# Kernel tuning notes

Measured on AMD Instinct MI355X. Metric: run time of the kernel, lower is better.

Reference implementation:

```python
import jax, jax.numpy as jnp
import numpy as np

N_NODES = 50000
N_EDGES = 800000
FEAT = 64
HID = 128
N_TYPES = 4
N_REL = 3
N_LAYERS = 2
LN_EPS = 1e-5


def setup_inputs() -> dict:
    key = jax.random.key(0)
    ks = jax.random.split(key, 20)
    inp = {
        "z": jax.random.randint(ks[0], (N_NODES,), 0, 100, dtype=jnp.int32),
        "node_type": jax.random.randint(ks[1], (N_NODES,), 0, N_TYPES, dtype=jnp.int32),
        "edge_index": jax.random.randint(ks[2], (2, N_EDGES), 0, N_NODES, dtype=jnp.int32),
        "edge_type": jax.random.randint(ks[3], (N_EDGES,), 0, N_REL, dtype=jnp.int32),
        # learned parameters
        "z_embed": jax.random.normal(ks[4], (100, FEAT), jnp.float32),
        "enc_w1": jax.random.normal(ks[5], (N_TYPES, FEAT, HID), jnp.float32) * 0.05,
        "enc_b1": jnp.zeros((N_TYPES, HID), jnp.float32),
        "enc_w2": jax.random.normal(ks[6], (N_TYPES, HID, HID), jnp.float32) * 0.05,
        "enc_b2": jnp.zeros((N_TYPES, HID), jnp.float32),
        "lin_w": jax.random.normal(ks[7], (N_LAYERS, HID, HID), jnp.float32) * 0.05,
        "lin_b": jnp.zeros((N_LAYERS, HID), jnp.float32),
        "rel_w": jax.random.normal(ks[8], (N_LAYERS, N_REL, HID, HID), jnp.float32) * 0.05,
        "ln_g": jnp.ones((N_LAYERS, HID), jnp.float32),
        "ln_b": jnp.zeros((N_LAYERS, HID), jnp.float32),
        "reg_w": jax.random.normal(ks[9], (HID, 1), jnp.float32) * 0.05,
        "reg_b": jnp.zeros((1,), jnp.float32),
    }
    return inp


def _layer_norm(x, g, b):
    mu = jnp.mean(x, axis=-1, keepdims=True)
    var = jnp.mean((x - mu) ** 2, axis=-1, keepdims=True)
    return (x - mu) * jax.lax.rsqrt(var + LN_EPS) * g + b


def reference(z, node_type, edge_index, edge_type, z_embed, enc_w1, enc_b1,
              enc_w2, enc_b2, lin_w, lin_b, rel_w, ln_g, ln_b, reg_w, reg_b):
    n = z.shape[0]
    # FeatureBuilder (site_ads=None path): atomic-number embedding lookup
    raw = z_embed[z]  # [N, FEAT]
    # TypeSpecificEncoder: run all 4 type MLPs, select per node by node_type
    h = jax.nn.relu(jnp.einsum('nd,tdh->nth', raw, enc_w1) + enc_b1)  # [N,T,H]
    enc_all = jnp.einsum('nth,tho->nto', h, enc_w2) + enc_b2           # [N,T,H]
    x = jnp.take_along_axis(enc_all, node_type[:, None, None].astype(jnp.int32), axis=1)[:, 0, :]

    src, dst = edge_index[0], edge_index[1]
    deg = jax.ops.segment_sum(jnp.ones((edge_type.shape[0],), x.dtype), dst, num_segments=n)
    deg = jnp.clip(deg, 1.0, None)[:, None]  # [N,1]

    for l in range(N_LAYERS):
        out = jnp.zeros_like(x)
        x_src = x[src]  # [E, H] gathered source features
        for r in range(N_REL):
            mask = (edge_type == r).astype(x.dtype)[:, None]
            msg = (x_src * mask) @ rel_w[l, r]  # [E, H]
            out = out + jax.ops.segment_sum(msg, dst, num_segments=n)
        out = out / deg
        x = _layer_norm(x @ lin_w[l] + lin_b[l] + out, ln_g[l], ln_b[l])

    pooled = jnp.mean(x, axis=0)  # mean pooling, mask = all ones
    return pooled @ reg_w + reg_b  # [1]
```

## Files before the change

### kernel.cpp

```cpp
#include <hip/hip_runtime.h>

#define N_NODES 50000
#define N_EDGES 800000
#define FEAT 64
#define HID 128
#define N_TYPES 4
#define N_REL 3
#define N_LAYERS 2
#define LN_EPS 1e-5f
#define NROWS 50016
#define NG32 1563
#define CAP 64
#define NBKT 196
#define CAP1 4608
#define EPB 4096
#define BINCAP 56
#define NCOMBO 400
#define WT_STRIDE 136

typedef __attribute__((ext_vector_type(8))) short bf16x8;
typedef __attribute__((ext_vector_type(16))) float f32x16;
typedef __attribute__((ext_vector_type(2))) float f32x2;

static __device__ inline unsigned short f2bf(float f) {
    unsigned int u = __float_as_uint(f);
    return (unsigned short)((u + 0x7fffu + ((u >> 16) & 1u)) >> 16);
}
static __device__ inline unsigned int packbf2(float lo, float hi) {
    return (unsigned int)f2bf(lo) | ((unsigned int)f2bf(hi) << 16);
}

static __device__ inline void acc8_fp8(float* a, uint2 w) {
    f32x2 d0 = __builtin_amdgcn_cvt_pk_f32_fp8((int)w.x, false);
    f32x2 d1 = __builtin_amdgcn_cvt_pk_f32_fp8((int)w.x, true);
    f32x2 d2 = __builtin_amdgcn_cvt_pk_f32_fp8((int)w.y, false);
    f32x2 d3 = __builtin_amdgcn_cvt_pk_f32_fp8((int)w.y, true);
    a[0] += d0[0]; a[1] += d0[1]; a[2] += d1[0]; a[3] += d1[1];
    a[4] += d2[0]; a[5] += d2[1]; a[6] += d3[0]; a[7] += d3[1];
}
static __device__ inline bf16x8 f8_to_bf16x8(uint2 w) {
    f32x2 d0 = __builtin_amdgcn_cvt_pk_f32_fp8((int)w.x, false);
    f32x2 d1 = __builtin_amdgcn_cvt_pk_f32_fp8((int)w.x, true);
    f32x2 d2 = __builtin_amdgcn_cvt_pk_f32_fp8((int)w.y, false);
    f32x2 d3 = __builtin_amdgcn_cvt_pk_f32_fp8((int)w.y, true);
    union { bf16x8 v; unsigned int u[4]; } r;
    r.u[0] = packbf2(d0[0], d0[1]);
    r.u[1] = packbf2(d1[0], d1[1]);
    r.u[2] = packbf2(d2[0], d2[1]);
    r.u[3] = packbf2(d3[0], d3[1]);
    return r.v;
}

__global__ __launch_bounds__(256) void build_tables_kernel(
    const int* __restrict__ src, const int* __restrict__ dst,
    const int* __restrict__ et, const int* __restrict__ z,
    const int* __restrict__ nt,
    const float* __restrict__ z_embed, const float* __restrict__ w1,
    const float* __restrict__ b1, const float* __restrict__ w2,
    const float* __restrict__ b2, const float* __restrict__ rel_w,
    const float* __restrict__ lin_w, const float* __restrict__ lin_b,
    unsigned short* __restrict__ combo, int* __restrict__ bcnt,
    int* __restrict__ bucket, unsigned int* __restrict__ ytab,
    float* __restrict__ lintab, unsigned short* __restrict__ wbuf,
    float* __restrict__ pooled) {
    __shared__ int lbin[NBKT * BINCAP];
    __shared__ int lcnt[NBKT];
    __shared__ int lbase[NBKT];
    __shared__ float h[HID];
    __shared__ float xrow[HID];
    __shared__ float tmp[HID];

    int b = blockIdx.x;
    if (b < NBKT) {
        int ci = b * 256 + threadIdx.x;
        if (ci < N_NODES) combo[ci] = (unsigned short)(z[ci] * 4 + nt[ci]);
        for (int i = threadIdx.x; i < NBKT; i += 256) lcnt[i] = 0;
        __syncthreads();
        int base = b * EPB;
#pragma unroll
        for (int i = 0; i < EPB / 256; ++i) {
            int e = base + i * 256 + threadIdx.x;
            if (e < N_EDGES) {
                int d = dst[e];
                int bk = d >> 8;
                int v = src[e] | (et[e] << 16) | ((d & 255) << 18);
                int pos = atomicAdd(&lcnt[bk], 1);
                if (pos < BINCAP) lbin[bk * BINCAP + pos] = v;
            }
        }
        __syncthreads();
        if (threadIdx.x < NBKT) {
            int c = min(lcnt[threadIdx.x], BINCAP);
            lcnt[threadIdx.x] = c;
            lbase[threadIdx.x] = atomicAdd(&bcnt[threadIdx.x], c);
        }
        __syncthreads();
        int wv = threadIdx.x >> 6, ln = threadIdx.x & 63;
        for (int bb = wv; bb < NBKT; bb += 4) {
            int c = lcnt[bb];
            if (ln < c) {
                int gp = lbase[bb] + ln;
                if (gp < CAP1) bucket[bb * CAP1 + gp] = lbin[bb * BINCAP + ln];
            }
        }
        return;
    }
    if (b >= NBKT + NCOMBO) {
        int pb = b - (NBKT + NCOMBO);
        if (pb == 0 && threadIdx.x < HID) pooled[threadIdx.x] = 0.0f;
        int idx = pb * 256 + threadIdx.x;
        int k = idx & 127;
        int col = (idx >> 7) & 127;
        int mat = idx >> 14;
        float w = (mat < 3) ? rel_w[(((size_t)(3 + mat)) * HID + k) * HID + col]
                            : lin_w[((size_t)(HID + k)) * HID + col];
        wbuf[(size_t)mat * HID * WT_STRIDE + col * WT_STRIDE + k] = f2bf(w);
        return;
    }
    int c = b - NBKT;
    int zi = c >> 2;
    int t = c & 3;
    int j = threadIdx.x;
    bool act = j < HID;
    if (act) {
        float acc = b1[t * HID + j];
#pragma unroll 8
        for (int k = 0; k < FEAT; ++k)
            acc = fmaf(z_embed[zi * FEAT + k], w1[((size_t)t * FEAT + k) * HID + j], acc);
        h[j] = fmaxf(acc, 0.0f);
    }
    __syncthreads();
    if (act) {
        float acc2 = b2[t * HID + j];
#pragma unroll 8
        for (int k = 0; k < HID; ++k)
            acc2 = fmaf(h[k], w2[(size_t)t * HID * HID + k * HID + j], acc2);
        xrow[j] = acc2;
    }
    __syncthreads();
#pragma unroll 1
    for (int r = 0; r < N_REL; ++r) {
        if (act) {
            float a = 0.f;
            const float* W = rel_w + (size_t)r * HID * HID;
#pragma unroll 8
            for (int k = 0; k < HID; ++k) a = fmaf(xrow[k], W[k * HID + j], a);
            tmp[j] = a;
        }
        __syncthreads();
        if (j < 32) {
            int w0 = __builtin_amdgcn_cvt_pk_fp8_f32(tmp[4 * j], tmp[4 * j + 1], 0, false);
            w0 = __builtin_amdgcn_cvt_pk_fp8_f32(tmp[4 * j + 2], tmp[4 * j + 3], w0, true);
            ytab[(r * NCOMBO + c) * 32 + j] = (unsigned)w0;
        }
        __syncthreads();
    }
    if (act) {
        float a = lin_b[j];
#pragma unroll 8
        for (int k = 0; k < HID; ++k) a = fmaf(xrow[k], lin_w[k * HID + j], a);
        lintab[c * HID + j] = a;
    }
}

__global__ __launch_bounds__(256) void build2_kernel(const int* __restrict__ bcnt,
                                                     const int* __restrict__ bucket,
                                                     const unsigned short* __restrict__ combo,
                                                     int* __restrict__ cnt3,
                                                     int* __restrict__ payload) {
    __shared__ int lcnt[256 * 3];
    for (int i = threadIdx.x; i < 768; i += 256) lcnt[i] = 0;
    __syncthreads();
    int b = blockIdx.x;
    int n0 = b << 8;
    int cb = min(bcnt[b], CAP1);
    const int* bk = bucket + b * CAP1;
    for (int i = threadIdx.x; i < cb; i += 256) {
        int v = bk[i];
        atomicAdd(&lcnt[((v >> 18) & 255) * 3 + ((v >> 16) & 3)], 1);
    }
    __syncthreads();
    int t = threadIdx.x;
    int c0 = min(lcnt[t * 3 + 0], CAP);
    int c1 = min(lcnt[t * 3 + 1], CAP - c0);
    int c2 = min(lcnt[t * 3 + 2], CAP - c0 - c1);
    __syncthreads();
    lcnt[t * 3 + 0] = 0;
    lcnt[t * 3 + 1] = c0;
    lcnt[t * 3 + 2] = c0 + c1;
    int node = n0 + t;
    if (node < N_NODES) cnt3[node] = c0 | (c1 << 8) | (c2 << 16);
    __syncthreads();
    for (int i = threadIdx.x; i < cb; i += 256) {
        int v = bk[i];
        int dl = (v >> 18) & 255;
        int r = (v >> 16) & 3;
        int sc = v & 0xffff;
        int pos = atomicAdd(&lcnt[dl * 3 + r], 1);
        if (pos < CAP)
            payload[((n0 + dl) << 6) + pos] = sc | ((int)combo[sc] << 18);
    }
}

__global__ __launch_bounds__(256) void gather_ln1_kernel(
    const int* __restrict__ cnt3, const int* __restrict__ payload,
    const uint2* __restrict__ ytab8, const float* __restrict__ lintab,
    const unsigned short* __restrict__ combo, const float* __restrict__ lng,
    const float* __restrict__ lnb, uint2* __restrict__ xf8) {
    int tid = blockIdx.x * 256 + threadIdx.x;
    int node = tid >> 4;
    int l16 = tid & 15;
    int c3 = cnt3[node];
    int c0 = c3 & 255, c1 = (c3 >> 8) & 255, c2 = (c3 >> 16) & 255;
    int tot = c0 + c1 + c2;
    float inv = 1.0f / (float)max(tot, 1);
    const int* pl = payload + (node << 6);
    float a[8] = {};
    int e = 0;
#pragma unroll 1
    for (int r = 0; r < 3; ++r) {
        int e1 = (r == 0) ? c0 : (r == 1) ? c0 + c1 : tot;
        int base = (r * NCOMBO) << 4;
        for (; e + 4 <= e1; e += 4) {
            int pA = pl[e], pB = pl[e + 1], pC = pl[e + 2], pD = pl[e + 3];
            uint2 vA = ytab8[base + ((pA >> 18) << 4) + l16];
            uint2 vB = ytab8[base + ((pB >> 18) << 4) + l16];
            uint2 vC = ytab8[base + ((pC >> 18) << 4) + l16];
            uint2 vD = ytab8[base + ((pD >> 18) << 4) + l16];
            acc8_fp8(a, vA);
            acc8_fp8(a, vB);
            acc8_fp8(a, vC);
            acc8_fp8(a, vD);
        }
        if (e + 2 <= e1) {
            int pA = pl[e], pB = pl[e + 1];
            uint2 vA = ytab8[base + ((pA >> 18) << 4) + l16];
            uint2 vB = ytab8[base + ((pB >> 18) << 4) + l16];
            acc8_fp8(a, vA);
            acc8_fp8(a, vB);
            e += 2;
        }
        if (e < e1) {
            int p = pl[e]; ++e;
            acc8_fp8(a, ytab8[base + ((p >> 18) << 4) + l16]);
        }
    }
    const float* lrow = lintab + (int)combo[node] * HID + l16 * 8;
    float v[8], s = 0.f, q = 0.f;
#pragma unroll
    for (int j = 0; j < 8; ++j) {
        v[j] = fmaf(a[j], inv, lrow[j]);
        s += v[j];
        q += v[j] * v[j];
    }
#pragma unroll
    for (int mk = 1; mk < 16; mk <<= 1) {
        s += __shfl_xor(s, mk);
        q += __shfl_xor(q, mk);
    }
    float mu = s * (1.0f / HID);
    float rstd = rsqrtf(q * (1.0f / HID) - mu * mu + LN_EPS);
    const float* g8 = lng + l16 * 8;
    const float* b8 = lnb + l16 * 8;
    float o[8];
#pragma unroll
    for (int j = 0; j < 8; ++j) o[j] = (v[j] - mu) * rstd * g8[j] + b8[j];
    int lo = 0, hi = 0;
    lo = __builtin_amdgcn_cvt_pk_fp8_f32(o[0], o[1], lo, false);
    lo = __builtin_amdgcn_cvt_pk_fp8_f32(o[2], o[3], lo, true);
    hi = __builtin_amdgcn_cvt_pk_fp8_f32(o[4], o[5], hi, false);
    hi = __builtin_amdgcn_cvt_pk_fp8_f32(o[6], o[7], hi, true);
    xf8[(node << 4) + l16] = make_uint2((unsigned)lo, (unsigned)hi);
}

__global__ __launch_bounds__(256) void gather3_kernel(const int* __restrict__ cnt3,
                                                      const int* __restrict__ payload,
                                                      const uint2* __restrict__ xf8,
                                                      uint2* __restrict__ s0,
                                                      uint2* __restrict__ s1,
                                                      uint2* __restrict__ s2) {
    int tid = blockIdx.x * 256 + threadIdx.x;
    int node = tid >> 4;
    int l16 = tid & 15;
    int c3 = cnt3[node];
    int c0 = c3 & 255, c1 = (c3 >> 8) & 255, c2 = (c3 >> 16) & 255;
    int tot = c0 + c1 + c2;
    float inv = 1.0f / (float)max(tot, 1);
    const int* pl = payload + (node << 6);
    int o = node * 16 + l16;
    int e = 0;
#pragma unroll 1
    for (int r = 0; r < 3; ++r) {
        int e1 = (r == 0) ? c0 : (r == 1) ? c0 + c1 : tot;
        float a[8] = {};
        for (; e + 4 <= e1; e += 4) {
            int pA = pl[e], pB = pl[e + 1], pC = pl[e + 2], pD = pl[e + 3];
            uint2 vA = xf8[((pA & 0xffff) << 4) + l16];
            uint2 vB = xf8[((pB & 0xffff) << 4) + l16];
            uint2 vC = xf8[((pC & 0xffff) << 4) + l16];
            uint2 vD = xf8[((pD & 0xffff) << 4) + l16];
            acc8_fp8(a, vA);
            acc8_fp8(a, vB);
            acc8_fp8(a, vC);
            acc8_fp8(a, vD);
        }
        if (e + 2 <= e1) {
            int pA = pl[e], pB = pl[e + 1];
            uint2 vA = xf8[((pA & 0xffff) << 4) + l16];
            uint2 vB = xf8[((pB & 0xffff) << 4) + l16];
            acc8_fp8(a, vA);
            acc8_fp8(a, vB);
            e += 2;
        }
        if (e < e1) {
            int p = pl[e]; ++e;
            acc8_fp8(a, xf8[((p & 0xffff) << 4) + l16]);
        }
        int lo = 0, hi = 0;
        lo = __builtin_amdgcn_cvt_pk_fp8_f32(a[0] * inv, a[1] * inv, lo, false);
        lo = __builtin_amdgcn_cvt_pk_fp8_f32(a[2] * inv, a[3] * inv, lo, true);
        hi = __builtin_amdgcn_cvt_pk_fp8_f32(a[4] * inv, a[5] * inv, hi, false);
        hi = __builtin_amdgcn_cvt_pk_fp8_f32(a[6] * inv, a[7] * inv, hi, true);
        uint2 w = make_uint2((unsigned)lo, (unsigned)hi);
        if (r == 0) s0[o] = w;
        else if (r == 1) s1[o] = w;
        else s2[o] = w;
    }
}

__global__ __launch_bounds__(512) void fused_layer_kernel(
    const uint2* __restrict__ s0, const uint2* __restrict__ s1,
    const uint2* __restrict__ s2, const uint2* __restrict__ xf8,
    const uint4* __restrict__ wbuf, const float* __restrict__ lb,
    const float* __restrict__ lng, const float* __restrict__ lnb,
    float* __restrict__ pooled, const float* __restrict__ reg_w,
    const float* __restrict__ reg_b, float* __restrict__ out,
    int* __restrict__ done) {
    __shared__ __align__(16) unsigned short Wt[4 * HID * WT_STRIDE];
    __shared__ float csh[3 * HID];
    __shared__ float pooled_sh[HID];
    __shared__ int lastFlag;

    int wave = threadIdx.x >> 6;
    int lane = threadIdx.x & 63;
    int n32 = lane & 31;
    int hf = lane >> 5;

    int g0 = wave * gridDim.x + blockIdx.x;
    bool active = g0 < NG32;
    int rbase = active ? ((g0 * 32 + n32) * 16 + hf) : 0;

    uint2 bufA[8], bufB[8];
    {
        const uint2* p0 = s0 + rbase;
#pragma unroll
        for (int t = 0; t < 8; ++t) bufA[t] = p0[t * 2];
    }

    if (threadIdx.x < HID) {
        pooled_sh[threadIdx.x] = 0.0f;
        csh[threadIdx.x] = lb[threadIdx.x];
        csh[HID + threadIdx.x] = lng[threadIdx.x];
        csh[2 * HID + threadIdx.x] = lnb[threadIdx.x];
    }
    uint4* wt4 = (uint4*)Wt;
#pragma unroll
    for (int i = 0; i < 17; ++i)
        wt4[i * 512 + threadIdx.x] = wbuf[i * 512 + threadIdx.x];
    __syncthreads();

    float pacc[4] = {0.f, 0.f, 0.f, 0.f};

    if (active) {
        f32x16 acc[4];
#pragma unroll
        for (int ct = 0; ct < 4; ++ct)
#pragma unroll
            for (int i = 0; i < 16; ++i) acc[ct][i] = 0.0f;

        const unsigned short* wbase = Wt + n32 * WT_STRIDE + hf * 8;

#define DOMAT(buf, m)                                                          \
        {                                                                      \
            const unsigned short* wm = wbase + (m) * (HID * WT_STRIDE);        \
            _Pragma("unroll")                                                  \
            for (int t = 0; t < 8; ++t) {                                      \
                bf16x8 afr = f8_to_bf16x8(buf[t]);                             \
                _Pragma("unroll")                                              \
                for (int ct = 0; ct < 4; ++ct) {                               \
                    bf16x8 bfr = *(const bf16x8*)(wm + ct * 32 * WT_STRIDE + t * 16); \
                    acc[ct] = __builtin_amdgcn_mfma_f32_32x32x16_bf16(         \
                        afr, bfr, acc[ct], 0, 0, 0);                           \
                }                                                              \
            }                                                                  \
        }
#define LDMAT(buf, srcp)                                                       \
        {                                                                      \
            const uint2* _p = (srcp) + rbase;                                  \
            _Pragma("unroll")                                                  \
            for (int t = 0; t < 8; ++t) buf[t] = _p[t * 2];                    \
        }

        LDMAT(bufB, s1);
        DOMAT(bufA, 0);
        LDMAT(bufA, s2);
        DOMAT(bufB, 1);
        LDMAT(bufB, xf8);
        DOMAT(bufA, 2);
        DOMAT(bufB, 3);
#undef DOMAT
#undef LDMAT

        int node0 = g0 * 32;
#pragma unroll
        for (int reg = 0; reg < 16; ++reg) {
            int row = node0 + (reg & 3) + 8 * (reg >> 2) + 4 * hf;
            float v[4];
            float s = 0.f, q = 0.f;
#pragma unroll
            for (int ct = 0; ct < 4; ++ct) {
                v[ct] = acc[ct][reg] + csh[ct * 32 + n32];
                s += v[ct];
                q += v[ct] * v[ct];
            }
#pragma unroll
            for (int mk = 1; mk < 32; mk <<= 1) {
                s += __shfl_xor(s, mk);
                q += __shfl_xor(q, mk);
            }
            float mu = s * (1.0f / HID);
            float rstd = rsqrtf(q * (1.0f / HID) - mu * mu + LN_EPS);
            if (row < N_NODES) {
#pragma unroll
                for (int ct = 0; ct < 4; ++ct) {
                    int col = ct * 32 + n32;
                    pacc[ct] += (v[ct] - mu) * rstd * csh[HID + col] + csh[2 * HID + col];
                }
            }
        }
    }

#pragma unroll
    for (int ct = 0; ct < 4; ++ct) {
        float t = pacc[ct] + __shfl_xor(pacc[ct], 32);
        if (hf == 0) atomicAdd(&pooled_sh[ct * 32 + n32], t);
    }
    __syncthreads();
    if (threadIdx.x < HID) atomicAdd(&pooled[threadIdx.x], pooled_sh[threadIdx.x]);

    __threadfence();
    __syncthreads();
    if (threadIdx.x == 0)
        lastFlag = (atomicAdd(done, 1) == (int)gridDim.x - 1);
    __syncthreads();
    if (lastFlag && threadIdx.x < 64) {
        int l = threadIdx.x;
        float s = atomicAdd(&pooled[l], 0.0f) * reg_w[l] +
                  atomicAdd(&pooled[64 + l], 0.0f) * reg_w[64 + l];
#pragma unroll
        for (int o = 32; o; o >>= 1) s += __shfl_down(s, o);
        if (l == 0) out[0] = s * (1.0f / N_NODES) + reg_b[0];
    }
}

extern "C" void kernel_launch(void* const* d_in, const int* in_sizes, int n_in,
                              void* d_out, int out_size, void* d_ws, size_t ws_size,
                              hipStream_t stream) {
    const int* z = (const int*)d_in[0];
    const int* nt = (const int*)d_in[1];
    const int* ei = (const int*)d_in[2];
    const int* et = (const int*)d_in[3];
    const float* z_embed = (const float*)d_in[4];
    const float* enc_w1 = (const float*)d_in[5];
    const float* enc_b1 = (const float*)d_in[6];
    const float* enc_w2 = (const float*)d_in[7];
    const float* enc_b2 = (const float*)d_in[8];
    const float* lin_w = (const float*)d_in[9];
    const float* lin_b = (const float*)d_in[10];
    const float* rel_w = (const float*)d_in[11];
    const float* ln_g = (const float*)d_in[12];
    const float* ln_b = (const float*)d_in[13];
    const float* reg_w = (const float*)d_in[14];
    const float* reg_b = (const float*)d_in[15];
    float* out = (float*)d_out;

    const size_t NHf8 = (size_t)NROWS * HID;
    char* p = (char*)d_ws;
    uint2* xf8 = (uint2*)p;                     p += NHf8;
    uint2* s0 = (uint2*)p;                      p += NHf8;
    uint2* s1 = (uint2*)p;                      p += NHf8;
    uint2* s2 = (uint2*)p;                      p += NHf8;
    unsigned short* wbuf = (unsigned short*)p;  p += (size_t)4 * HID * WT_STRIDE * 2;
    unsigned int* ytab = (unsigned int*)p;      p += (size_t)N_REL * NCOMBO * HID;
    float* lintab = (float*)p;                  p += NCOMBO * HID * 4;
    unsigned short* combo = (unsigned short*)p; p += N_NODES * 2;
    float* pooled = (float*)p;                  p += HID * 4;
    int* cnt3 = (int*)p;                        p += N_NODES * 4;
    int* bcnt = (int*)p;                        p += NBKT * 4;
    int* done = (int*)p;                        p += 4;
    int* bucket = (int*)p;                      p += (size_t)NBKT * CAP1 * 4;
    int* payload = (int*)p;                     p += (size_t)N_NODES * CAP * 4;

    const int* src = ei;
    const int* dst = ei + N_EDGES;

    hipMemsetAsync(bcnt, 0, (NBKT + 1) * sizeof(int), stream);

    build_tables_kernel<<<NBKT + NCOMBO + 256, 256, 0, stream>>>(
        src, dst, et, z, nt, z_embed, enc_w1, enc_b1, enc_w2, enc_b2,
        rel_w, lin_w, lin_b, combo, bcnt, bucket, ytab, lintab, wbuf, pooled);

    build2_kernel<<<NBKT, 256, 0, stream>>>(bcnt, bucket, combo, cnt3, payload);

    gather_ln1_kernel<<<3125, 256, 0, stream>>>(cnt3, payload, (const uint2*)ytab, lintab,
                                                combo, ln_g, ln_b, xf8);
    gather3_kernel<<<3125, 256, 0, stream>>>(cnt3, payload, xf8, s0, s1, s2);
    fused_layer_kernel<<<256, 512, 0, stream>>>(
        s0, s1, s2, xf8, (const uint4*)wbuf, lin_b + HID, ln_g + HID, ln_b + HID,
        pooled, reg_w, reg_b, out, done);
}
```

Baseline: 230.2 us.

## Permute fp8 row layout for 16-byte loads and read weights from global

```diff
diff --git a/kernel.cpp b/kernel.cpp
--- a/kernel.cpp
+++ b/kernel.cpp
@@ -270,7 +270,8 @@
     lo = __builtin_amdgcn_cvt_pk_fp8_f32(o[2], o[3], lo, true);
     hi = __builtin_amdgcn_cvt_pk_fp8_f32(o[4], o[5], hi, false);
     hi = __builtin_amdgcn_cvt_pk_fp8_f32(o[6], o[7], hi, true);
-    xf8[(node << 4) + l16] = make_uint2((unsigned)lo, (unsigned)hi);
+    int slot = (l16 >> 1) + ((l16 & 1) << 3);
+    xf8[(node << 4) + slot] = make_uint2((unsigned)lo, (unsigned)hi);
 }
 
 __global__ __launch_bounds__(256) void gather3_kernel(const int* __restrict__ cnt3,
@@ -282,12 +283,13 @@
     int tid = blockIdx.x * 256 + threadIdx.x;
     int node = tid >> 4;
     int l16 = tid & 15;
+    int slot = (l16 >> 1) + ((l16 & 1) << 3);
     int c3 = cnt3[node];
     int c0 = c3 & 255, c1 = (c3 >> 8) & 255, c2 = (c3 >> 16) & 255;
     int tot = c0 + c1 + c2;
     float inv = 1.0f / (float)max(tot, 1);
     const int* pl = payload + (node << 6);
-    int o = node * 16 + l16;
+    int o = node * 16 + slot;
     int e = 0;
 #pragma unroll 1
     for (int r = 0; r < 3; ++r) {
@@ -295,10 +297,10 @@
         float a[8] = {};
         for (; e + 4 <= e1; e += 4) {
             int pA = pl[e], pB = pl[e + 1], pC = pl[e + 2], pD = pl[e + 3];
-            uint2 vA = xf8[((pA & 0xffff) << 4) + l16];
-            uint2 vB = xf8[((pB & 0xffff) << 4) + l16];
-            uint2 vC = xf8[((pC & 0xffff) << 4) + l16];
-            uint2 vD = xf8[((pD & 0xffff) << 4) + l16];
+            uint2 vA = xf8[((pA & 0xffff) << 4) + slot];
+            uint2 vB = xf8[((pB & 0xffff) << 4) + slot];
+            uint2 vC = xf8[((pC & 0xffff) << 4) + slot];
+            uint2 vD = xf8[((pD & 0xffff) << 4) + slot];
             acc8_fp8(a, vA);
             acc8_fp8(a, vB);
             acc8_fp8(a, vC);
@@ -306,15 +308,15 @@
         }
         if (e + 2 <= e1) {
             int pA = pl[e], pB = pl[e + 1];
-            uint2 vA = xf8[((pA & 0xffff) << 4) + l16];
-            uint2 vB = xf8[((pB & 0xffff) << 4) + l16];
+            uint2 vA = xf8[((pA & 0xffff) << 4) + slot];
+            uint2 vB = xf8[((pB & 0xffff) << 4) + slot];
             acc8_fp8(a, vA);
             acc8_fp8(a, vB);
             e += 2;
         }
         if (e < e1) {
             int p = pl[e]; ++e;
-            acc8_fp8(a, xf8[((p & 0xffff) << 4) + l16]);
+            acc8_fp8(a, xf8[((p & 0xffff) << 4) + slot]);
         }
         int lo = 0, hi = 0;
         lo = __builtin_amdgcn_cvt_pk_fp8_f32(a[0] * inv, a[1] * inv, lo, false);
@@ -329,14 +331,13 @@
 }
 
 __global__ __launch_bounds__(512) void fused_layer_kernel(
-    const uint2* __restrict__ s0, const uint2* __restrict__ s1,
-    const uint2* __restrict__ s2, const uint2* __restrict__ xf8,
-    const uint4* __restrict__ wbuf, const float* __restrict__ lb,
+    const uint4* __restrict__ s0, const uint4* __restrict__ s1,
+    const uint4* __restrict__ s2, const uint4* __restrict__ xf8,
+    const unsigned short* __restrict__ wbuf, const float* __restrict__ lb,
     const float* __restrict__ lng, const float* __restrict__ lnb,
     float* __restrict__ pooled, const float* __restrict__ reg_w,
     const float* __restrict__ reg_b, float* __restrict__ out,
     int* __restrict__ done) {
-    __shared__ __align__(16) unsigned short Wt[4 * HID * WT_STRIDE];
     __shared__ float csh[3 * HID];
     __shared__ float pooled_sh[HID];
     __shared__ int lastFlag;
@@ -348,13 +349,14 @@
 
     int g0 = wave * gridDim.x + blockIdx.x;
     bool active = g0 < NG32;
-    int rbase = active ? ((g0 * 32 + n32) * 16 + hf) : 0;
-
-    uint2 bufA[8], bufB[8];
+    int abase = active ? ((g0 * 32 + n32) * 8 + hf * 4) : 0;
+
+    uint4 bufA[4], bufB[4];
     {
-        const uint2* p0 = s0 + rbase;
-#pragma unroll
-        for (int t = 0; t < 8; ++t) bufA[t] = p0[t * 2];
+        const uint4* p0 = s0 + abase;
+        const uint4* p1 = s1 + abase;
+#pragma unroll
+        for (int i = 0; i < 4; ++i) { bufA[i] = p0[i]; bufB[i] = p1[i]; }
     }
 
     if (threadIdx.x < HID) {
@@ -363,10 +365,6 @@
         csh[HID + threadIdx.x] = lng[threadIdx.x];
         csh[2 * HID + threadIdx.x] = lnb[threadIdx.x];
     }
-    uint4* wt4 = (uint4*)Wt;
-#pragma unroll
-    for (int i = 0; i < 17; ++i)
-        wt4[i * 512 + threadIdx.x] = wbuf[i * 512 + threadIdx.x];
     __syncthreads();
 
     float pacc[4] = {0.f, 0.f, 0.f, 0.f};
@@ -378,14 +376,16 @@
 #pragma unroll
             for (int i = 0; i < 16; ++i) acc[ct][i] = 0.0f;
 
-        const unsigned short* wbase = Wt + n32 * WT_STRIDE + hf * 8;
+        const unsigned short* wlane = wbuf + n32 * WT_STRIDE + hf * 8;
 
 #define DOMAT(buf, m)                                                          \
         {                                                                      \
-            const unsigned short* wm = wbase + (m) * (HID * WT_STRIDE);        \
+            const unsigned short* wm = wlane + (size_t)(m) * (HID * WT_STRIDE);\
             _Pragma("unroll")                                                  \
             for (int t = 0; t < 8; ++t) {                                      \
-                bf16x8 afr = f8_to_bf16x8(buf[t]);                             \
+                uint2 f = (t & 1) ? make_uint2(buf[t >> 1].z, buf[t >> 1].w)   \
+                                  : make_uint2(buf[t >> 1].x, buf[t >> 1].y);  \
+                bf16x8 afr = f8_to_bf16x8(f);                                  \
                 _Pragma("unroll")                                              \
                 for (int ct = 0; ct < 4; ++ct) {                               \
                     bf16x8 bfr = *(const bf16x8*)(wm + ct * 32 * WT_STRIDE + t * 16); \
@@ -396,12 +396,11 @@
         }
 #define LDMAT(buf, srcp)                                                       \
         {                                                                      \
-            const uint2* _p = (srcp) + rbase;                                  \
+            const uint4* _p = (srcp) + abase;                                  \
             _Pragma("unroll")                                                  \
-            for (int t = 0; t < 8; ++t) buf[t] = _p[t * 2];                    \
-        }
-
-        LDMAT(bufB, s1);
+            for (int i = 0; i < 4; ++i) buf[i] = _p[i];                        \
+        }
+
         DOMAT(bufA, 0);
         LDMAT(bufA, s2);
         DOMAT(bufB, 1);
@@ -443,7 +442,7 @@
 #pragma unroll
     for (int ct = 0; ct < 4; ++ct) {
         float t = pacc[ct] + __shfl_xor(pacc[ct], 32);
-        if (hf == 0) atomicAdd(&pooled_sh[ct * 32 + n32], t);
+        if (hf == 0 && t != 0.0f) atomicAdd(&pooled_sh[ct * 32 + n32], t);
     }
     __syncthreads();
     if (threadIdx.x < HID) atomicAdd(&pooled[threadIdx.x], pooled_sh[threadIdx.x]);
@@ -515,7 +514,8 @@
     gather_ln1_kernel<<<3125, 256, 0, stream>>>(cnt3, payload, (const uint2*)ytab, lintab,
                                                 combo, ln_g, ln_b, xf8);
     gather3_kernel<<<3125, 256, 0, stream>>>(cnt3, payload, xf8, s0, s1, s2);
-    fused_layer_kernel<<<256, 512, 0, stream>>>(
-        s0, s1, s2, xf8, (const uint4*)wbuf, lin_b + HID, ln_g + HID, ln_b + HID,
+    fused_layer_kernel<<<784, 512, 0, stream>>>(
+        (const uint4*)s0, (const uint4*)s1, (const uint4*)s2, (const uint4*)xf8,
+        wbuf, lin_b + HID, ln_g + HID, ln_b + HID,
         pooled, reg_w, reg_b, out, done);
 }
```

After: 331.2 us. 1.44x slower.

## Switch final layer to 16x16x32 MFMA tiles with two groups per wave

Applied to the files above, without the earlier changes.

```diff
diff --git a/kernel.cpp b/kernel.cpp
--- a/kernel.cpp
+++ b/kernel.cpp
@@ -9,7 +9,7 @@
 #define N_LAYERS 2
 #define LN_EPS 1e-5f
 #define NROWS 50016
-#define NG32 1563
+#define NG16 3125
 #define CAP 64
 #define NBKT 196
 #define CAP1 4608
@@ -19,7 +19,7 @@
 #define WT_STRIDE 136
 
 typedef __attribute__((ext_vector_type(8))) short bf16x8;
-typedef __attribute__((ext_vector_type(16))) float f32x16;
+typedef __attribute__((ext_vector_type(4))) float f32x4;
 typedef __attribute__((ext_vector_type(2))) float f32x2;
 
 static __device__ inline unsigned short f2bf(float f) {
@@ -343,19 +343,25 @@
 
     int wave = threadIdx.x >> 6;
     int lane = threadIdx.x & 63;
-    int n32 = lane & 31;
-    int hf = lane >> 5;
+    int c16 = lane & 15;
+    int kg = lane >> 4;
 
     int g0 = wave * gridDim.x + blockIdx.x;
-    bool active = g0 < NG32;
-    int rbase = active ? ((g0 * 32 + n32) * 16 + hf) : 0;
-
-    uint2 bufA[8], bufB[8];
-    {
-        const uint2* p0 = s0 + rbase;
-#pragma unroll
-        for (int t = 0; t < 8; ++t) bufA[t] = p0[t * 2];
-    }
+    uint2 buf[16];
+
+#define LDALL(g)                                                               \
+    {                                                                          \
+        int _b = ((g) * 16 + c16) * 16 + kg;  \
+        _Pragma("unroll")                                                      \
+        for (int kk = 0; kk < 4; ++kk) {                                       \
+            buf[0 * 4 + kk] = s0[_b + kk * 4];                                 \
+            buf[1 * 4 + kk] = s1[_b + kk * 4];                                 \
+            buf[2 * 4 + kk] = s2[_b + kk * 4];                                 \
+            buf[3 * 4 + kk] = xf8[_b + kk * 4];                                \
+        }                                                                      \
+    }
+
+    LDALL(g0);
 
     if (threadIdx.x < HID) {
         pooled_sh[threadIdx.x] = 0.0f;
@@ -369,81 +375,75 @@
         wt4[i * 512 + threadIdx.x] = wbuf[i * 512 + threadIdx.x];
     __syncthreads();
 
-    float pacc[4] = {0.f, 0.f, 0.f, 0.f};
-
-    if (active) {
-        f32x16 acc[4];
-#pragma unroll
-        for (int ct = 0; ct < 4; ++ct)
-#pragma unroll
-            for (int i = 0; i < 16; ++i) acc[ct][i] = 0.0f;
-
-        const unsigned short* wbase = Wt + n32 * WT_STRIDE + hf * 8;
-
-#define DOMAT(buf, m)                                                          \
-        {                                                                      \
-            const unsigned short* wm = wbase + (m) * (HID * WT_STRIDE);        \
+    float pacc[8] = {};
+    const unsigned short* wlane = Wt + c16 * WT_STRIDE + kg * 8;
+
+#define COMPUTE(accv)                                                          \
+    _Pragma("unroll")                                                          \
+    for (int mat = 0; mat < 4; ++mat) {                                        \
+        const unsigned short* wm = wlane + mat * (HID * WT_STRIDE);            \
+        _Pragma("unroll")                                                      \
+        for (int kk = 0; kk < 4; ++kk) {                                       \
+            bf16x8 afr = f8_to_bf16x8(buf[mat * 4 + kk]);                      \
             _Pragma("unroll")                                                  \
-            for (int t = 0; t < 8; ++t) {                                      \
-                bf16x8 afr = f8_to_bf16x8(buf[t]);                             \
-                _Pragma("unroll")                                              \
-                for (int ct = 0; ct < 4; ++ct) {                               \
-                    bf16x8 bfr = *(const bf16x8*)(wm + ct * 32 * WT_STRIDE + t * 16); \
-                    acc[ct] = __builtin_amdgcn_mfma_f32_32x32x16_bf16(         \
-                        afr, bfr, acc[ct], 0, 0, 0);                           \
-                }                                                              \
+            for (int tile = 0; tile < 8; ++tile) {                             \
+                bf16x8 bfr = *(const bf16x8*)(wm + tile * 16 * WT_STRIDE + kk * 32); \
+                accv[tile] = __builtin_amdgcn_mfma_f32_16x16x32_bf16(          \
+                    afr, bfr, accv[tile], 0, 0, 0);                            \
             }                                                                  \
-        }
-#define LDMAT(buf, srcp)                                                       \
-        {                                                                      \
-            const uint2* _p = (srcp) + rbase;                                  \
-            _Pragma("unroll")                                                  \
-            for (int t = 0; t < 8; ++t) buf[t] = _p[t * 2];                    \
-        }
-
-        LDMAT(bufB, s1);
-        DOMAT(bufA, 0);
-        LDMAT(bufA, s2);
-        DOMAT(bufB, 1);
-        LDMAT(bufB, xf8);
-        DOMAT(bufA, 2);
-        DOMAT(bufB, 3);
-#undef DOMAT
-#undef LDMAT
-
-        int node0 = g0 * 32;
-#pragma unroll
-        for (int reg = 0; reg < 16; ++reg) {
-            int row = node0 + (reg & 3) + 8 * (reg >> 2) + 4 * hf;
-            float v[4];
-            float s = 0.f, q = 0.f;
-#pragma unroll
-            for (int ct = 0; ct < 4; ++ct) {
-                v[ct] = acc[ct][reg] + csh[ct * 32 + n32];
-                s += v[ct];
-                q += v[ct] * v[ct];
-            }
-#pragma unroll
-            for (int mk = 1; mk < 32; mk <<= 1) {
-                s += __shfl_xor(s, mk);
-                q += __shfl_xor(q, mk);
-            }
-            float mu = s * (1.0f / HID);
-            float rstd = rsqrtf(q * (1.0f / HID) - mu * mu + LN_EPS);
-            if (row < N_NODES) {
-#pragma unroll
-                for (int ct = 0; ct < 4; ++ct) {
-                    int col = ct * 32 + n32;
-                    pacc[ct] += (v[ct] - mu) * rstd * csh[HID + col] + csh[2 * HID + col];
-                }
-            }
-        }
-    }
-
-#pragma unroll
-    for (int ct = 0; ct < 4; ++ct) {
-        float t = pacc[ct] + __shfl_xor(pacc[ct], 32);
-        if (hf == 0) atomicAdd(&pooled_sh[ct * 32 + n32], t);
+        }                                                                      \
+    }
+
+#define EPILOGUE(accv)                                                         \
+    _Pragma("unroll")                                                          \
+    for (int reg = 0; reg < 4; ++reg) {                                        \
+        float v[8], s = 0.f, q = 0.f;                                          \
+        _Pragma("unroll")                                                      \
+        for (int tile = 0; tile < 8; ++tile) {                                 \
+            v[tile] = accv[tile][reg] + csh[tile * 16 + c16];                  \
+            s += v[tile];                                                      \
+            q += v[tile] * v[tile];                                            \
+        }                                                                      \
+        _Pragma("unroll")                                                      \
+        for (int mk = 1; mk < 16; mk <<= 1) {                                  \
+            s += __shfl_xor(s, mk);                                            \
+            q += __shfl_xor(q, mk);                                            \
+        }                                                                      \
+        float mu = s * (1.0f / HID);                                           \
+        float rstd = rsqrtf(q * (1.0f / HID) - mu * mu + LN_EPS);              \
+        _Pragma("unroll")                                                      \
+        for (int tile = 0; tile < 8; ++tile) {                                 \
+            int col = tile * 16 + c16;                                         \
+            pacc[tile] += (v[tile] - mu) * rstd * csh[HID + col] + csh[2 * HID + col]; \
+        }                                                                      \
+    }
+
+    {
+        f32x4 acc[8];
+#pragma unroll
+        for (int t = 0; t < 8; ++t) acc[t] = (f32x4){0.f, 0.f, 0.f, 0.f};
+        COMPUTE(acc);
+        int g1 = g0 + 2048;
+        bool has2 = g1 < NG16;
+        if (has2) LDALL(g1);
+        EPILOGUE(acc);
+        if (has2) {
+            f32x4 acc2[8];
+#pragma unroll
+            for (int t = 0; t < 8; ++t) acc2[t] = (f32x4){0.f, 0.f, 0.f, 0.f};
+            COMPUTE(acc2);
+            EPILOGUE(acc2);
+        }
+    }
+#undef LDALL
+#undef COMPUTE
+#undef EPILOGUE
+
+#pragma unroll
+    for (int tile = 0; tile < 8; ++tile) {
+        float t = pacc[tile] + __shfl_xor(pacc[tile], 16);
+        t += __shfl_xor(t, 32);
+        if (kg == 0) atomicAdd(&pooled_sh[tile * 16 + c16], t);
     }
     __syncthreads();
     if (threadIdx.x < HID) atomicAdd(&pooled[threadIdx.x], pooled_sh[threadIdx.x]);
```

Result: no change. 232.9 us (+1.2%).
